# Performance work log

Hardware: AMD Instinct MI355X
Metric: run time of the kernel (lower is better)

Reference implementation:

```python
import jax, jax.numpy as jnp
import numpy as np

G = 8           # graphs
NBG = 1024      # blocks per graph
APB = 4         # atoms per block
NC = 1          # coord channels
HID = 512
ES = 64
K = 9
L = 3
NLVL = 50
NB = G * NBG
NU = NB * APB
NUM_BLOCK, NUM_ATOM, NUM_POS = 25, 16, 16
BIG = 1e9


def _cumsum_ids(seg_lengths, n):
    # faithful to torch: zeros, mark segment starts via cumsum(lengths)[:-1], cumsum
    ids = jnp.zeros((n,), jnp.int32).at[jnp.cumsum(seg_lengths)[:-1]].set(1)
    return jnp.cumsum(ids)


def setup_inputs() -> dict:
    key = jax.random.key(0)
    ks = jax.random.split(key, 18)
    s = 0.02
    return {
        'Z': 3.0 * jax.random.normal(ks[0], (NU, NC, 3), jnp.float32),
        'B': jax.random.randint(ks[1], (NB,), 0, NUM_BLOCK),
        'A': jax.random.randint(ks[2], (NU,), 0, NUM_ATOM),
        'atom_positions': jax.random.randint(ks[3], (NU,), 0, NUM_POS),
        'block_lengths': jnp.full((NB,), APB, jnp.int32),
        'lengths': jnp.full((G,), NBG, jnp.int32),
        'segment_ids': jax.random.randint(ks[4], (NB,), 0, 2),
        'noise': jax.random.normal(ks[5], (NU, NC, 3), jnp.float32),
        'noise_level': jax.random.randint(ks[6], (G,), 0, NLVL),
        'sigmas': jnp.asarray(np.exp(np.linspace(np.log(10.0), np.log(0.01), NLVL)), jnp.float32),
        'atom_emb': s * jax.random.normal(ks[7], (NUM_ATOM, HID), jnp.float32),
        'pos_emb': s * jax.random.normal(ks[8], (NUM_POS, HID), jnp.float32),
        'block_emb': s * jax.random.normal(ks[9], (NUM_BLOCK, HID), jnp.float32),
        'edge_emb': s * jax.random.normal(ks[10], (2, ES), jnp.float32),
        'Wm': s * jax.random.normal(ks[11], (L, HID, HID), jnp.float32),
        'We': s * jax.random.normal(ks[12], (L, ES, HID), jnp.float32),
        'Wu': s * jax.random.normal(ks[13], (L, HID, HID), jnp.float32),
        'wz': s * jax.random.normal(ks[14], (L, HID), jnp.float32),
        'W1': s * jax.random.normal(ks[15], (HID, HID), jnp.float32),
        'b1': jnp.zeros((HID,), jnp.float32),
        'W2': s * jax.random.normal(ks[16], (HID, 1), jnp.float32),
    }


def _forward(Z, B, A, atom_positions, block_lengths, lengths, segment_ids,
             noise, noise_level, sigmas, atom_emb, pos_emb, block_emb, edge_emb,
             Wm, We, Wu, wz, W1, b1, W2):
    nb, nu, g = B.shape[0], A.shape[0], lengths.shape[0]
    nbg, apb = nb // g, nu // nb
    batch_id = _cumsum_ids(lengths, nb)        # [Nb]
    block_id = _cumsum_ids(block_lengths, nu)  # [Nu]

    # perturb: Z + noise * sigma[noise_level[graph]]
    used = sigmas[noise_level][batch_id][block_id]          # [Nu]
    Zp = Z + noise * used[:, None, None]                    # [Nu, NC, 3]

    # block embedding: atom + position + block-type
    H0 = atom_emb[A] + pos_emb[atom_positions] + block_emb[B][block_id]  # [Nu, H]

    # edges: fully connect -> split intra/inter by segment -> knn by min atom-pair distance
    xa = Zp.reshape(g, nbg * apb * NC, 3)
    sq = jnp.sum(xa * xa, axis=-1)
    d2 = sq[:, :, None] + sq[:, None, :] - 2.0 * jnp.einsum('gnd,gmd->gnm', xa, xa)
    D = d2.reshape(g, nbg, apb * NC, nbg, apb * NC).min(axis=(2, 4))     # [g, nbg, nbg]
    seg = segment_ids.reshape(g, nbg)
    same = seg[:, :, None] == seg[:, None, :]
    eye = jnp.eye(nbg, dtype=bool)[None]
    _, idx_intra = jax.lax.top_k(-jnp.where(same & ~eye, D, BIG), K)     # [g, nbg, K]
    _, idx_inter = jax.lax.top_k(-jnp.where(~same, D, BIG), K)
    off = (jnp.arange(g, dtype=jnp.int32) * nbg)[:, None, None]
    dst_loc = jnp.broadcast_to(jnp.arange(nbg, dtype=jnp.int32)[None, :, None] + off, (g, nbg, K))
    src = jnp.concatenate([(idx_intra + off).reshape(-1), (idx_inter + off).reshape(-1)])
    dst = jnp.concatenate([dst_loc.reshape(-1), dst_loc.reshape(-1)])
    eattr = edge_emb[jnp.concatenate([jnp.zeros(g * nbg * K, jnp.int32), jnp.ones(g * nbg * K, jnp.int32)])]

    # encoder (GET surrogate): block-level equivariant message passing
    h = jax.ops.segment_sum(H0, block_id, num_segments=nb) / apb                    # [Nb, H]
    Zb0 = jax.ops.segment_sum(Zp.mean(axis=1), block_id, num_segments=nb) / apb    # [Nb, 3]
    Zb = Zb0
    for l in range(Wm.shape[0]):
        m = jax.nn.silu((h[src] + h[dst]) @ Wm[l] + eattr @ We[l])                  # [E, H]
        h = h + jax.nn.silu(jax.ops.segment_sum(m, dst, num_segments=nb) @ Wu[l])
        coef = jnp.tanh(m @ wz[l])                                                  # [E]
        Zb = Zb + jax.ops.segment_sum((Zb[src] - Zb[dst]) * coef[:, None], dst, num_segments=nb) / (2 * K)
    pred_Z = Zp + (Zb - Zb0)[block_id][:, None, :]
    unit_repr = H0 + h[block_id]
    block_repr = h
    graph_repr = jax.ops.segment_sum(h, batch_id, num_segments=g)

    # energy head: SiLU -> Linear -> SiLU -> Linear(no bias), summed per graph
    e = jax.nn.silu(jax.nn.silu(block_repr) @ W1 + b1) @ W2                         # [Nb, 1]
    pred_energy = jax.ops.segment_sum(e[:, 0], batch_id, num_segments=g)            # [g]

    pred_noise = pred_Z - Zp
    per_unit = jnp.sum((pred_noise - noise) ** 2, axis=(-1, -2))                    # [Nu]
    nl = jax.ops.segment_sum(per_unit, batch_id[block_id], num_segments=g)
    loss = 0.5 * nl.mean()
    return pred_energy, pred_noise, unit_repr, block_repr, graph_repr, loss


def reference(Z, B, A, atom_positions, block_lengths, lengths, segment_ids,
              noise, noise_level, sigmas, atom_emb, pos_emb, block_emb, edge_emb,
              Wm, We, Wu, wz, W1, b1, W2):
    return _forward(Z, B, A, atom_positions, block_lengths, lengths, segment_ids,
                    noise, noise_level, sigmas, atom_emb, pos_emb, block_emb, edge_emb,
                    Wm, We, Wu, wz, W1, b1, W2)
```

## Files before the change

kernel.cpp:

```cpp
#include <hip/hip_runtime.h>
#include <hip/hip_bf16.h>

typedef __bf16 bf16;
typedef __bf16 bf16x2 __attribute__((ext_vector_type(2)));
typedef __bf16 bf16x8 __attribute__((ext_vector_type(8)));
typedef float floatx4 __attribute__((ext_vector_type(4)));

#define NB_ 8192
#define NU_ 32768

__device__ __forceinline__ float silu_f(float x) {
    float e = __expf(-x);
    return x * __builtin_amdgcn_rcpf(1.0f + e);
}

__device__ __forceinline__ float2 unpack_bf2(unsigned v) {
    float2 r;
    r.x = __uint_as_float(v << 16);
    r.y = __uint_as_float(v & 0xFFFF0000u);
    return r;
}

__device__ __forceinline__ void gll16(const bf16* g, bf16* l) {
    __builtin_amdgcn_global_load_lds((const __attribute__((address_space(1))) void*)g,
                                     (__attribute__((address_space(3))) void*)l, 16, 0, 0);
}

__global__ __launch_bounds__(256) void init_kernel(
    const float* __restrict__ Z, const float* __restrict__ noise,
    const int* __restrict__ nl, const float* __restrict__ sig,
    const int* __restrict__ Aarr, const int* __restrict__ posa, const int* __restrict__ Barr,
    const float* __restrict__ atom_emb, const float* __restrict__ pos_emb,
    const float* __restrict__ block_emb,
    const float* __restrict__ edge_emb, const float* __restrict__ We,
    const float* __restrict__ Wm, const float* __restrict__ Wu, const float* __restrict__ W1,
    float* __restrict__ Zp, float* __restrict__ Zb0, float* __restrict__ Zb,
    float* __restrict__ hf, bf16* __restrict__ hb,
    bf16* __restrict__ WmT, bf16* __restrict__ WuT, bf16* __restrict__ W1T,
    float* __restrict__ ebias,
    float* __restrict__ out_gr, float* __restrict__ out_e, float* __restrict__ out_loss)
{
    __shared__ float zsh[12];
    __shared__ float tile[32][33];
    int bid = blockIdx.x, tid = threadIdx.x;
    if (bid < 8192) {
        int b = bid, g = b >> 10;
        if (tid < 12) {
            float sg = sig[nl[g]];
            int idx = b*12 + tid;
            float zp = Z[idx] + noise[idx]*sg;
            Zp[idx] = zp;
            zsh[tid] = zp;
        }
        __syncthreads();
        if (tid < 3) {
            float v = 0.25f*(zsh[tid] + zsh[3+tid] + zsh[6+tid] + zsh[9+tid]);
            Zb0[b*3+tid] = v; Zb[b*3+tid] = v;
        }
        int ai[4], pi[4];
        #pragma unroll
        for (int a = 0; a < 4; a++) { ai[a] = Aarr[b*4+a]*512; pi[a] = posa[b*4+a]*512; }
        int bb = Barr[b]*512;
        int c0 = tid*2;
        float sx = 0.0f, sy = 0.0f;
        #pragma unroll
        for (int a = 0; a < 4; a++) {
            float2 va = *(const float2*)(atom_emb + ai[a] + c0);
            float2 vp = *(const float2*)(pos_emb + pi[a] + c0);
            sx += va.x + vp.x; sy += va.y + vp.y;
        }
        float2 vb = *(const float2*)(block_emb + bb + c0);
        sx = 0.25f*sx + vb.x; sy = 0.25f*sy + vb.y;
        *(float2*)(hf + (size_t)b*512 + c0) = make_float2(sx, sy);
        bf16x2 hp = { (bf16)sx, (bf16)sy };
        *(bf16x2*)(hb + (size_t)b*512 + c0) = hp;
        return;
    }
    bid -= 8192;
    if (bid < 1792) {
        int z = bid >> 8, rem = bid & 255;
        int bx = rem & 15, by = rem >> 4;
        int tx = tid & 31, ty = tid >> 5;
        const float* src; bf16* dst;
        if (z < 3)      { src = Wm + (size_t)z*262144;     dst = WmT + (size_t)z*262144; }
        else if (z < 6) { src = Wu + (size_t)(z-3)*262144; dst = WuT + (size_t)(z-3)*262144; }
        else            { src = W1;                        dst = W1T; }
        #pragma unroll
        for (int i = 0; i < 32; i += 8)
            tile[ty+i][tx] = src[(size_t)(by*32+ty+i)*512 + bx*32+tx];
        __syncthreads();
        #pragma unroll
        for (int i = 0; i < 32; i += 8)
            dst[(size_t)(bx*32+ty+i)*512 + by*32+tx] = (bf16)tile[tx][ty+i];
        return;
    }
    bid -= 1792;
    if (bid < 12) {
        int gid = bid*256 + tid;
        int l = gid >> 10, t = (gid >> 9) & 1, c = gid & 511;
        float s = 0.0f;
        #pragma unroll 8
        for (int e = 0; e < 64; e++)
            s += edge_emb[t*64 + e] * We[(size_t)(l*64 + e)*512 + c];
        ebias[gid] = s;
        return;
    }
    bid -= 12;
    int k = bid*256 + tid;
    if (k < 4096) out_gr[k] = 0.0f;
    else if (k < 4104) out_e[k-4096] = 0.0f;
    else if (k == 4104) out_loss[0] = 0.0f;
}

__device__ void knn_body(int kb, const float* __restrict__ Zp, const int* __restrict__ seg,
                         int* __restrict__ nbr, unsigned* __restrict__ l1) {
    int tid = threadIdx.x, w = tid >> 6, lane = tid & 63;
    int g = kb & 7, rl = kb >> 3;
    int r = (g << 10) + rl;
    int base = g << 10;
    int segr = seg[r];
    const float4* zp4 = (const float4*)(Zp + (size_t)r*12);
    float4 a0 = zp4[0], a1 = zp4[1], a2 = zp4[2];
    float ax[4] = {a0.x, a0.w, a1.z, a2.y};
    float ay[4] = {a0.y, a1.x, a1.w, a2.z};
    float az[4] = {a0.z, a1.y, a2.x, a2.w};
    unsigned kin[4], kout[4];
    #pragma unroll
    for (int t = 0; t < 4; t++) {
        int j = w*256 + t*64 + lane;
        int jb = base + j;
        const float4* p = (const float4*)(Zp + (size_t)jb*12);
        float4 v0 = p[0], v1 = p[1], v2 = p[2];
        float bx[4] = {v0.x, v0.w, v1.z, v2.y};
        float by[4] = {v0.y, v1.x, v1.w, v2.z};
        float bz[4] = {v0.z, v1.y, v2.x, v2.w};
        float dm = 3.0e38f;
        #pragma unroll
        for (int a = 0; a < 4; a++) {
            #pragma unroll
            for (int bq = 0; bq < 4; bq++) {
                float dx = ax[a]-bx[bq], dy = ay[a]-by[bq], dz = az[a]-bz[bq];
                dm = fminf(dm, dx*dx + dy*dy + dz*dz);
            }
        }
        unsigned kd = (__float_as_uint(dm) & 0xFFFFFC00u) | (unsigned)j;
        bool same = (seg[jb] == segr);
        kin[t]  = (same && j != rl) ? kd : 0xFFFFFFFFu;
        kout[t] = (!same)           ? kd : 0xFFFFFFFFu;
    }
    if (tid < 128) l1[tid] = 0xFFFFFFFFu;
    __syncthreads();
    #pragma unroll
    for (int ph = 0; ph < 2; ph++) {
        unsigned wd[4];
        #pragma unroll
        for (int t = 0; t < 4; t++) wd[t] = ph ? kout[t] : kin[t];
        for (int it = 0; it < 9; it++) {
            unsigned bk = min(min(wd[0], wd[1]), min(wd[2], wd[3]));
            unsigned mv = bk;
            #pragma unroll
            for (int off = 32; off >= 1; off >>= 1)
                mv = min(mv, (unsigned)__shfl_xor((int)mv, off, 64));
            if (lane == 0) l1[ph*64 + w*16 + it] = mv;
            if (bk == mv) {
                #pragma unroll
                for (int t = 0; t < 4; t++) if (wd[t] == mv) wd[t] = 0xFFFFFFFFu;
            }
        }
    }
    __syncthreads();
    if (w < 2) {
        int ph = w;
        int w2 = lane >> 4, it2 = lane & 15;
        unsigned key = (it2 < 9) ? l1[ph*64 + w2*16 + it2] : 0xFFFFFFFFu;
        for (int it = 0; it < 9; it++) {
            unsigned mv = key;
            #pragma unroll
            for (int off = 32; off >= 1; off >>= 1)
                mv = min(mv, (unsigned)__shfl_xor((int)mv, off, 64));
            if (key == mv) key = 0xFFFFFFFFu;
            if (lane == 0) nbr[r*18 + ph*9 + it] = base + (int)(mv & 1023u);
        }
    }
}

__device__ void gemm_body(const bf16* __restrict__ A, const bf16* __restrict__ BT,
                          bf16* __restrict__ Pb, float* __restrict__ hf,
                          bf16* __restrict__ hb, bf16* __restrict__ shp,
                          const float* __restrict__ b1, const float* __restrict__ W2,
                          float* __restrict__ out_e,
                          float* __restrict__ Zb, const float* __restrict__ zacc,
                          int mode, int bid, bf16* __restrict__ sA, bf16* __restrict__ sB)
{
    int mt = bid & 127, nt = bid >> 7;
    int m0 = mt*64, n0 = nt*64;
    int tid = threadIdx.x, lane = tid & 63, w = tid >> 6;
    int wm = w & 1, wn = w >> 1;
    int lm = lane & 15, q = lane >> 4;

    int row = tid >> 2;
    int qt = (tid & 3) ^ ((row >> 1) & 3);
    const bf16* gA = A  + (size_t)(m0 + row)*512 + qt*8;
    const bf16* gB = BT + (size_t)(n0 + row)*512 + qt*8;
    bf16* lA = sA + tid*8 - lane*8;
    bf16* lB = sB + tid*8 - lane*8;
    int swq = (q ^ ((lm >> 1) & 3)) * 8;

    floatx4 zv = {0.0f, 0.0f, 0.0f, 0.0f};
    floatx4 acc[2][2];
    #pragma unroll
    for (int i = 0; i < 2; i++)
        #pragma unroll
        for (int j = 0; j < 2; j++) acc[i][j] = zv;

    gll16(gA, lA);
    gll16(gB, lB);
    for (int k = 0; k < 16; k++) {
        int cur = (k & 1)*2048;
        __syncthreads();
        if (k < 15) {
            int nxt = ((k+1) & 1)*2048;
            gll16(gA + (k+1)*32, lA + nxt);
            gll16(gB + (k+1)*32, lB + nxt);
        }
        const bf16* bA = sA + cur;
        const bf16* bB = sB + cur;
        bf16x8 af[2], bfr[2];
        af[0]  = *(const bf16x8*)(bA + (wm*32      + lm)*32 + swq);
        af[1]  = *(const bf16x8*)(bA + (wm*32 + 16 + lm)*32 + swq);
        bfr[0] = *(const bf16x8*)(bB + (wn*32      + lm)*32 + swq);
        bfr[1] = *(const bf16x8*)(bB + (wn*32 + 16 + lm)*32 + swq);
        #pragma unroll
        for (int tm = 0; tm < 2; tm++)
            #pragma unroll
            for (int tn = 0; tn < 2; tn++)
                acc[tm][tn] = __builtin_amdgcn_mfma_f32_16x16x32_bf16(af[tm], bfr[tn], acc[tm][tn], 0, 0, 0);
    }

    if (mode == 2) {
        float s = 0.0f;
        #pragma unroll
        for (int tn = 0; tn < 2; tn++) {
            int col = n0 + wn*32 + tn*16 + lm;
            float bb = b1[col], ww = W2[col];
            #pragma unroll
            for (int tm = 0; tm < 2; tm++)
                #pragma unroll
                for (int rr = 0; rr < 4; rr++)
                    s += silu_f(acc[tm][tn][rr] + bb) * ww;
        }
        #pragma unroll
        for (int off = 32; off >= 1; off >>= 1) s += __shfl_xor(s, off, 64);
        if (lane == 0) atomicAdd(&out_e[m0 >> 10], s);
        return;
    }
    if (mode == 1 && nt == 0 && tid < 192) {
        int o = m0*3 + tid;
        Zb[o] += zacc[o] * (1.0f/18.0f);
    }
    #pragma unroll
    for (int tm = 0; tm < 2; tm++) {
        #pragma unroll
        for (int tn = 0; tn < 2; tn++) {
            #pragma unroll
            for (int rr = 0; rr < 4; rr++) {
                int r2 = m0 + wm*32 + tm*16 + q*4 + rr;
                int c2 = n0 + wn*32 + tn*16 + lm;
                size_t o = (size_t)r2*512 + c2;
                float v = acc[tm][tn][rr];
                if (mode == 0) {
                    Pb[o] = (bf16)v;
                } else {
                    float nh = hf[o] + silu_f(v);
                    hf[o] = nh;
                    hb[o] = (bf16)nh;
                    if (shp) shp[o] = (bf16)silu_f(nh);
                }
            }
        }
    }
}

__global__ __launch_bounds__(256) void gemm_kernel(const bf16* __restrict__ A, const bf16* __restrict__ BT,
                                                   bf16* __restrict__ Pb, float* __restrict__ hf,
                                                   bf16* __restrict__ hb, bf16* __restrict__ shp,
                                                   float* __restrict__ Zb, const float* __restrict__ zacc,
                                                   int mode) {
    __shared__ __align__(16) char smem[16384];
    gemm_body(A, BT, Pb, hf, hb, shp, nullptr, nullptr, nullptr, Zb, zacc, mode, blockIdx.x,
              (bf16*)smem, (bf16*)(smem + 8192));
}

__global__ __launch_bounds__(256) void knn_pgemm0_kernel(const bf16* __restrict__ hb,
                                                         const bf16* __restrict__ WmT0,
                                                         bf16* __restrict__ Pb,
                                                         const float* __restrict__ Zp,
                                                         const int* __restrict__ seg,
                                                         int* __restrict__ nbr) {
    __shared__ __align__(16) char smem[16384];
    if (blockIdx.x < 8192)
        knn_body(blockIdx.x, Zp, seg, nbr, (unsigned*)smem);
    else
        gemm_body(hb, WmT0, Pb, nullptr, nullptr, nullptr, nullptr, nullptr, nullptr,
                  nullptr, nullptr, 0, blockIdx.x - 8192, (bf16*)smem, (bf16*)(smem + 8192));
}

__global__ __launch_bounds__(256) void edge_kernel(const bf16* __restrict__ Pb, const float* __restrict__ ebias,
                                                   const float* __restrict__ wz, const float* __restrict__ Zb,
                                                   const int* __restrict__ nbr, bf16* __restrict__ msum,
                                                   float* __restrict__ zacc) {
    int bid = blockIdx.x, tid = threadIdx.x;
    int b = ((bid & 7) << 10) | (bid >> 3);
    int c0 = 2*tid;
    int lane = tid & 63, wid = tid >> 6;
    __shared__ int srcs[18];
    __shared__ float red[18][4];
    __shared__ float term[18][3];
    if (tid < 18) srcs[tid] = nbr[b*18 + tid];
    __syncthreads();
    float2 pd  = unpack_bf2(*(const unsigned*)(Pb + (size_t)b*512 + c0));
    float2 eb0 = *(const float2*)(ebias + c0);
    float2 eb1 = *(const float2*)(ebias + 512 + c0);
    float2 w   = *(const float2*)(wz + c0);
    float ms0 = 0.0f, ms1 = 0.0f;
    float pdot[18];
    #pragma unroll
    for (int e = 0; e < 18; e++) {
        int s = srcs[e];
        float2 pv = unpack_bf2(*(const unsigned*)(Pb + (size_t)s*512 + c0));
        float ba = (e < 9) ? eb0.x : eb1.x;
        float bb = (e < 9) ? eb0.y : eb1.y;
        float m0 = silu_f(pv.x + pd.x + ba);
        float m1 = silu_f(pv.y + pd.y + bb);
        ms0 += m0; ms1 += m1;
        pdot[e] = m0*w.x + m1*w.y;
    }
    bf16x2 mp = { (bf16)ms0, (bf16)ms1 };
    *(bf16x2*)(msum + (size_t)b*512 + c0) = mp;
    #pragma unroll
    for (int e = 0; e < 18; e++) {
        float v = pdot[e];
        #pragma unroll
        for (int off = 32; off >= 1; off >>= 1) v += __shfl_xor(v, off, 64);
        if (lane == 0) red[e][wid] = v;
    }
    __syncthreads();
    if (tid < 18) {
        float dot = red[tid][0] + red[tid][1] + red[tid][2] + red[tid][3];
        float coef = tanhf(dot);
        int s = srcs[tid];
        #pragma unroll
        for (int d = 0; d < 3; d++)
            term[tid][d] = (Zb[s*3 + d] - Zb[b*3 + d]) * coef;
    }
    __syncthreads();
    if (tid < 3) {
        float s = 0.0f;
        #pragma unroll
        for (int e = 0; e < 18; e++) s += term[e][tid];
        zacc[b*3 + tid] = s;
    }
}

__global__ __launch_bounds__(256) void egemm_fin_kernel(const bf16* __restrict__ sh, const bf16* __restrict__ W1T,
                                                        const float* __restrict__ b1, const float* __restrict__ W2,
                                                        float* __restrict__ out_e,
                                                        const float* __restrict__ hf, float* __restrict__ out_gr,
                                                        const float* __restrict__ Zb, const float* __restrict__ Zb0,
                                                        const float* __restrict__ noise,
                                                        float* __restrict__ out_pn, float* __restrict__ out_loss) {
    __shared__ __align__(16) char smem[16384];
    int bid = blockIdx.x, tid = threadIdx.x;
    if (bid < 1024) {
        gemm_body(sh, W1T, nullptr, nullptr, nullptr, nullptr, b1, W2, out_e,
                  nullptr, nullptr, 2, bid, (bf16*)smem, (bf16*)(smem + 8192));
        return;
    }
    float* red = (float*)smem;
    if (bid < 1152) {
        int u = (bid-1024)*256 + tid;
        int b = u >> 2;
        float per = 0.0f;
        #pragma unroll
        for (int d = 0; d < 3; d++) {
            float dv = Zb[b*3+d] - Zb0[b*3+d];
            out_pn[u*3+d] = dv;
            float e = dv - noise[u*3+d];
            per += e*e;
        }
        red[tid] = per; __syncthreads();
        for (int st = 128; st > 0; st >>= 1) {
            if (tid < st) red[tid] += red[tid+st];
            __syncthreads();
        }
        if (tid == 0) atomicAdd(out_loss, red[0] * (1.0f/16.0f));
        return;
    }
    int pid = bid - 1152;
    int g = pid >> 5;
    int rc = (pid >> 1) & 15;
    int ch = pid & 1;
    int c = ch*256 + tid;
    int b0 = (g << 10) + rc*64;
    float s = 0.0f;
    for (int i = 0; i < 64; i++) s += hf[(size_t)(b0+i)*512 + c];
    atomicAdd(&out_gr[g*512 + c], s);
}

__global__ __launch_bounds__(256) void unitrepr_kernel(const int* __restrict__ Aarr, const int* __restrict__ posa,
                                                       const int* __restrict__ Barr,
                                                       const float* __restrict__ atom_emb, const float* __restrict__ pos_emb,
                                                       const float* __restrict__ block_emb,
                                                       const float* __restrict__ hf, float* __restrict__ out_ur) {
    int gid = blockIdx.x*256 + threadIdx.x;
    int u = gid >> 7, c = (gid & 127) << 2, b = u >> 2;
    float4 va = *(const float4*)(atom_emb + (size_t)Aarr[u]*512 + c);
    float4 vp = *(const float4*)(pos_emb + (size_t)posa[u]*512 + c);
    float4 vb = *(const float4*)(block_emb + (size_t)Barr[b]*512 + c);
    float4 vh = *(const float4*)(hf + (size_t)b*512 + c);
    float4 o;
    o.x = va.x + vp.x + vb.x + vh.x;
    o.y = va.y + vp.y + vb.y + vh.y;
    o.z = va.z + vp.z + vb.z + vh.z;
    o.w = va.w + vp.w + vb.w + vh.w;
    *(float4*)(out_ur + (size_t)u*512 + c) = o;
}

extern "C" void kernel_launch(void* const* d_in, const int* in_sizes, int n_in,
                              void* d_out, int out_size, void* d_ws, size_t ws_size,
                              hipStream_t stream) {
    const float* Z         = (const float*)d_in[0];
    const int*   B         = (const int*)d_in[1];
    const int*   A         = (const int*)d_in[2];
    const int*   ap        = (const int*)d_in[3];
    const int*   seg       = (const int*)d_in[6];
    const float* noise     = (const float*)d_in[7];
    const int*   nl        = (const int*)d_in[8];
    const float* sig       = (const float*)d_in[9];
    const float* atom_emb  = (const float*)d_in[10];
    const float* pos_emb   = (const float*)d_in[11];
    const float* block_emb = (const float*)d_in[12];
    const float* edge_emb  = (const float*)d_in[13];
    const float* Wm        = (const float*)d_in[14];
    const float* We        = (const float*)d_in[15];
    const float* Wu        = (const float*)d_in[16];
    const float* wz        = (const float*)d_in[17];
    const float* W1        = (const float*)d_in[18];
    const float* b1        = (const float*)d_in[19];
    const float* W2        = (const float*)d_in[20];
    (void)in_sizes; (void)n_in; (void)d_ws; (void)ws_size; (void)out_size;

    float* out = (float*)d_out;
    const size_t o1 = 8, o2 = 98312, o3 = 16875528, o4 = 21069832, o5 = 21073928;
    float* out_e    = out;
    float* out_pn   = out + o1;
    float* out_ur   = out + o2;
    float* hf       = out + o3;
    float* out_gr   = out + o4;
    float* out_loss = out + o5;

    char* arena = (char*)(out + o2);
    bf16*  Pb   = (bf16*)(arena);
    bf16*  msum = (bf16*)(arena + 16777216);
    bf16*  sh   = (bf16*)(arena + 25165824);
    bf16*  hb   = (bf16*)(arena + 33554432);
    float* Zp   = (float*)(arena + 41943040);
    float* Zb0  = (float*)(arena + 42336256);
    float* Zb   = (float*)(arena + 42434560);
    float* zacc = (float*)(arena + 42532864);
    int*   nbr  = (int*)  (arena + 42631168);
    bf16*  WmT  = (bf16*) (arena + 43220992);
    bf16*  WuT  = (bf16*) (arena + 44793856);
    bf16*  W1T  = (bf16*) (arena + 46366720);
    float* ebias= (float*)(arena + 46891008);

    init_kernel<<<8192 + 1792 + 12 + 17, 256, 0, stream>>>(
        Z, noise, nl, sig, A, ap, B, atom_emb, pos_emb, block_emb,
        edge_emb, We, Wm, Wu, W1,
        Zp, Zb0, Zb, hf, hb, WmT, WuT, W1T, ebias, out_gr, out_e, out_loss);

    knn_pgemm0_kernel<<<8192 + 1024, 256, 0, stream>>>(hb, WmT, Pb, Zp, seg, nbr);

    for (int l = 0; l < 3; l++) {
        if (l > 0)
            gemm_kernel<<<1024, 256, 0, stream>>>(hb, WmT + (size_t)l*262144, Pb,
                                                  nullptr, nullptr, nullptr, nullptr, nullptr, 0);
        edge_kernel<<<8192, 256, 0, stream>>>(Pb, ebias + l*1024, wz + l*512, Zb, nbr, msum, zacc);
        gemm_kernel<<<1024, 256, 0, stream>>>(msum, WuT + (size_t)l*262144, nullptr,
                                              hf, hb, (l == 2) ? sh : nullptr, Zb, zacc, 1);
    }
    egemm_fin_kernel<<<1024 + 128 + 256, 256, 0, stream>>>(sh, W1T, b1, W2, out_e,
                                                           hf, out_gr, Zb, Zb0, noise, out_pn, out_loss);
    unitrepr_kernel<<<16384, 256, 0, stream>>>(A, ap, B, atom_emb, pos_emb, block_emb, hf, out_ur);
}
```

Measured before the change: 530.2 us.

## Batch eight KNN queries per block and enlarge GEMM tile to 128x64

The KNN kernel now handles eight destination blocks per workgroup. Each candidate's coordinates and segment id are loaded once and reused across all eight queries, with distance keys and same-segment ballots staged in shared memory before each wave runs a top-9 selection for two queries. The GEMM body moves from a 64x64 to a 128x64 output tile, which halves the block count and improves operand reuse. In exchange it drops the double-buffered global-to-LDS prefetch for a single buffer with two barriers per k step, and it needs more registers and a larger shared allocation in the KNN kernel.

```diff
diff --git a/kernel.cpp b/kernel.cpp
--- a/kernel.cpp
+++ b/kernel.cpp
@@ -112,74 +112,94 @@
     else if (k == 4104) out_loss[0] = 0.0f;
 }
 
-__device__ void knn_body(int kb, const float* __restrict__ Zp, const int* __restrict__ seg,
-                         int* __restrict__ nbr, unsigned* __restrict__ l1) {
+__device__ void knn_body8(int kb, const float* __restrict__ Zp, const int* __restrict__ seg,
+                          int* __restrict__ nbr, char* __restrict__ smem) {
+    unsigned* keys = (unsigned*)smem;
+    unsigned* smk  = (unsigned*)(smem + 32768);
+    float*    dza  = (float*)(smem + 33792);
+    int*      sseg = (int*)(smem + 34176);
     int tid = threadIdx.x, w = tid >> 6, lane = tid & 63;
-    int g = kb & 7, rl = kb >> 3;
-    int r = (g << 10) + rl;
+    int g = kb & 7, grp = kb >> 3;
     int base = g << 10;
-    int segr = seg[r];
-    const float4* zp4 = (const float4*)(Zp + (size_t)r*12);
-    float4 a0 = zp4[0], a1 = zp4[1], a2 = zp4[2];
-    float ax[4] = {a0.x, a0.w, a1.z, a2.y};
-    float ay[4] = {a0.y, a1.x, a1.w, a2.z};
-    float az[4] = {a0.z, a1.y, a2.x, a2.w};
-    unsigned kin[4], kout[4];
+    int dst0 = grp << 3;
+    if (tid < 96) dza[tid] = Zp[(size_t)(base + dst0)*12 + tid];
+    if (tid < 8)  sseg[tid] = seg[base + dst0 + tid];
+    __syncthreads();
+    float sx[4][4], sy[4][4], sz[4][4]; int sj[4];
     #pragma unroll
     for (int t = 0; t < 4; t++) {
         int j = w*256 + t*64 + lane;
-        int jb = base + j;
-        const float4* p = (const float4*)(Zp + (size_t)jb*12);
+        const float4* p = (const float4*)(Zp + (size_t)(base + j)*12);
         float4 v0 = p[0], v1 = p[1], v2 = p[2];
-        float bx[4] = {v0.x, v0.w, v1.z, v2.y};
-        float by[4] = {v0.y, v1.x, v1.w, v2.z};
-        float bz[4] = {v0.z, v1.y, v2.x, v2.w};
-        float dm = 3.0e38f;
-        #pragma unroll
-        for (int a = 0; a < 4; a++) {
+        sx[t][0]=v0.x; sx[t][1]=v0.w; sx[t][2]=v1.z; sx[t][3]=v2.y;
+        sy[t][0]=v0.y; sy[t][1]=v1.x; sy[t][2]=v1.w; sy[t][3]=v2.z;
+        sz[t][0]=v0.z; sz[t][1]=v1.y; sz[t][2]=v2.x; sz[t][3]=v2.w;
+        sj[t] = seg[base + j];
+    }
+    #pragma unroll
+    for (int d = 0; d < 8; d++) {
+        const float4* ap4 = (const float4*)(dza + d*12);
+        float4 a0 = ap4[0], a1 = ap4[1], a2 = ap4[2];
+        float ax[4] = {a0.x, a0.w, a1.z, a2.y};
+        float ay[4] = {a0.y, a1.x, a1.w, a2.z};
+        float az[4] = {a0.z, a1.y, a2.x, a2.w};
+        int segd = sseg[d];
+        int dl = dst0 + d;
+        #pragma unroll
+        for (int t = 0; t < 4; t++) {
+            int j = w*256 + t*64 + lane;
+            float dm = 3.0e38f;
             #pragma unroll
-            for (int bq = 0; bq < 4; bq++) {
-                float dx = ax[a]-bx[bq], dy = ay[a]-by[bq], dz = az[a]-bz[bq];
-                dm = fminf(dm, dx*dx + dy*dy + dz*dz);
+            for (int a = 0; a < 4; a++) {
+                #pragma unroll
+                for (int bq = 0; bq < 4; bq++) {
+                    float dx = ax[a]-sx[t][bq], dy = ay[a]-sy[t][bq], dz = az[a]-sz[t][bq];
+                    dm = fminf(dm, dx*dx + dy*dy + dz*dz);
+                }
             }
-        }
-        unsigned kd = (__float_as_uint(dm) & 0xFFFFFC00u) | (unsigned)j;
-        bool same = (seg[jb] == segr);
-        kin[t]  = (same && j != rl) ? kd : 0xFFFFFFFFu;
-        kout[t] = (!same)           ? kd : 0xFFFFFFFFu;
-    }
-    if (tid < 128) l1[tid] = 0xFFFFFFFFu;
+            unsigned key = (__float_as_uint(dm) & 0xFFFFFC00u) | (unsigned)j;
+            if (j == dl) key = 0xFFFFFFFFu;
+            bool same = (sj[t] == segd);
+            unsigned long long bal = __ballot(same);
+            if (lane == 0) {
+                smk[d*32 + (w*4+t)*2]     = (unsigned)bal;
+                smk[d*32 + (w*4+t)*2 + 1] = (unsigned)(bal >> 32);
+            }
+            keys[d*1024 + j] = key;
+        }
+    }
     __syncthreads();
     #pragma unroll
-    for (int ph = 0; ph < 2; ph++) {
-        unsigned wd[4];
-        #pragma unroll
-        for (int t = 0; t < 4; t++) wd[t] = ph ? kout[t] : kin[t];
-        for (int it = 0; it < 9; it++) {
-            unsigned bk = min(min(wd[0], wd[1]), min(wd[2], wd[3]));
-            unsigned mv = bk;
+    for (int half = 0; half < 2; half++) {
+        int d = w + half*4;
+        int r = base + dst0 + d;
+        unsigned kk[16], sm[16];
+        #pragma unroll
+        for (int t2 = 0; t2 < 16; t2++) {
+            kk[t2] = keys[d*1024 + t2*64 + lane];
+            unsigned wrd = smk[d*32 + t2*2 + (lane >> 5)];
+            sm[t2] = (wrd >> (lane & 31)) & 1u;
+        }
+        #pragma unroll
+        for (int ph = 0; ph < 2; ph++) {
+            unsigned wd[16];
             #pragma unroll
-            for (int off = 32; off >= 1; off >>= 1)
-                mv = min(mv, (unsigned)__shfl_xor((int)mv, off, 64));
-            if (lane == 0) l1[ph*64 + w*16 + it] = mv;
-            if (bk == mv) {
+            for (int t2 = 0; t2 < 16; t2++)
+                wd[t2] = (ph == 0) ? (sm[t2] ? kk[t2] : 0xFFFFFFFFu)
+                                   : (sm[t2] ? 0xFFFFFFFFu : kk[t2]);
+            for (int it = 0; it < 9; it++) {
+                unsigned bk = wd[0];
                 #pragma unroll
-                for (int t = 0; t < 4; t++) if (wd[t] == mv) wd[t] = 0xFFFFFFFFu;
+                for (int t2 = 1; t2 < 16; t2++) bk = min(bk, wd[t2]);
+                unsigned mv = bk;
+                #pragma unroll
+                for (int off = 32; off >= 1; off >>= 1)
+                    mv = min(mv, (unsigned)__shfl_xor((int)mv, off, 64));
+                if (lane == 0) nbr[r*18 + ph*9 + it] = base + (int)(mv & 1023u);
+                #pragma unroll
+                for (int t2 = 0; t2 < 16; t2++)
+                    wd[t2] = (wd[t2] == mv) ? 0xFFFFFFFFu : wd[t2];
             }
-        }
-    }
-    __syncthreads();
-    if (w < 2) {
-        int ph = w;
-        int w2 = lane >> 4, it2 = lane & 15;
-        unsigned key = (it2 < 9) ? l1[ph*64 + w2*16 + it2] : 0xFFFFFFFFu;
-        for (int it = 0; it < 9; it++) {
-            unsigned mv = key;
-            #pragma unroll
-            for (int off = 32; off >= 1; off >>= 1)
-                mv = min(mv, (unsigned)__shfl_xor((int)mv, off, 64));
-            if (key == mv) key = 0xFFFFFFFFu;
-            if (lane == 0) nbr[r*18 + ph*9 + it] = base + (int)(mv & 1023u);
         }
     }
 }
@@ -192,49 +212,53 @@
                           float* __restrict__ Zb, const float* __restrict__ zacc,
                           int mode, int bid, bf16* __restrict__ sA, bf16* __restrict__ sB)
 {
-    int mt = bid & 127, nt = bid >> 7;
-    int m0 = mt*64, n0 = nt*64;
+    int mt = bid & 63, nt = bid >> 6;
+    int m0 = mt*128, n0 = nt*64;
     int tid = threadIdx.x, lane = tid & 63, w = tid >> 6;
     int wm = w & 1, wn = w >> 1;
     int lm = lane & 15, q = lane >> 4;
 
-    int row = tid >> 2;
-    int qt = (tid & 3) ^ ((row >> 1) & 3);
-    const bf16* gA = A  + (size_t)(m0 + row)*512 + qt*8;
-    const bf16* gB = BT + (size_t)(n0 + row)*512 + qt*8;
-    bf16* lA = sA + tid*8 - lane*8;
-    bf16* lB = sB + tid*8 - lane*8;
+    int pA0 = w*128 + lane, pA1 = pA0 + 64, pB = w*64 + lane;
+    int rA0 = pA0 >> 2, qA0 = (pA0 & 3) ^ ((rA0 >> 1) & 3);
+    int rA1 = pA1 >> 2, qA1 = (pA1 & 3) ^ ((rA1 >> 1) & 3);
+    int rB  = pB  >> 2, qB  = (pB  & 3) ^ ((rB  >> 1) & 3);
+    const bf16* gA0 = A  + (size_t)(m0 + rA0)*512 + qA0*8;
+    const bf16* gA1 = A  + (size_t)(m0 + rA1)*512 + qA1*8;
+    const bf16* gB  = BT + (size_t)(n0 + rB )*512 + qB*8;
+    bf16* lA0 = sA + (w*128)*8;
+    bf16* lA1 = sA + (w*128 + 64)*8;
+    bf16* lB  = sB + (w*64)*8;
+
     int swq = (q ^ ((lm >> 1) & 3)) * 8;
+    const bf16* pa[4]; const bf16* pb2[2];
+    #pragma unroll
+    for (int tm = 0; tm < 4; tm++) pa[tm] = sA + (wm*64 + tm*16 + lm)*32 + swq;
+    #pragma unroll
+    for (int tn = 0; tn < 2; tn++) pb2[tn] = sB + (wn*32 + tn*16 + lm)*32 + swq;
 
     floatx4 zv = {0.0f, 0.0f, 0.0f, 0.0f};
-    floatx4 acc[2][2];
-    #pragma unroll
-    for (int i = 0; i < 2; i++)
+    floatx4 acc[4][2];
+    #pragma unroll
+    for (int i = 0; i < 4; i++)
         #pragma unroll
         for (int j = 0; j < 2; j++) acc[i][j] = zv;
 
-    gll16(gA, lA);
-    gll16(gB, lB);
-    for (int k = 0; k < 16; k++) {
-        int cur = (k & 1)*2048;
+    for (int k0 = 0; k0 < 512; k0 += 32) {
+        gll16(gA0 + k0, lA0);
+        gll16(gA1 + k0, lA1);
+        gll16(gB  + k0, lB);
         __syncthreads();
-        if (k < 15) {
-            int nxt = ((k+1) & 1)*2048;
-            gll16(gA + (k+1)*32, lA + nxt);
-            gll16(gB + (k+1)*32, lB + nxt);
-        }
-        const bf16* bA = sA + cur;
-        const bf16* bB = sB + cur;
-        bf16x8 af[2], bfr[2];
-        af[0]  = *(const bf16x8*)(bA + (wm*32      + lm)*32 + swq);
-        af[1]  = *(const bf16x8*)(bA + (wm*32 + 16 + lm)*32 + swq);
-        bfr[0] = *(const bf16x8*)(bB + (wn*32      + lm)*32 + swq);
-        bfr[1] = *(const bf16x8*)(bB + (wn*32 + 16 + lm)*32 + swq);
-        #pragma unroll
-        for (int tm = 0; tm < 2; tm++)
+        bf16x8 af[4], bfr[2];
+        #pragma unroll
+        for (int tm = 0; tm < 4; tm++) af[tm] = *(const bf16x8*)pa[tm];
+        #pragma unroll
+        for (int tn = 0; tn < 2; tn++) bfr[tn] = *(const bf16x8*)pb2[tn];
+        #pragma unroll
+        for (int tm = 0; tm < 4; tm++)
             #pragma unroll
             for (int tn = 0; tn < 2; tn++)
                 acc[tm][tn] = __builtin_amdgcn_mfma_f32_16x16x32_bf16(af[tm], bfr[tn], acc[tm][tn], 0, 0, 0);
+        __syncthreads();
     }
 
     if (mode == 2) {
@@ -244,7 +268,7 @@
             int col = n0 + wn*32 + tn*16 + lm;
             float bb = b1[col], ww = W2[col];
             #pragma unroll
-            for (int tm = 0; tm < 2; tm++)
+            for (int tm = 0; tm < 4; tm++)
                 #pragma unroll
                 for (int rr = 0; rr < 4; rr++)
                     s += silu_f(acc[tm][tn][rr] + bb) * ww;
@@ -254,17 +278,21 @@
         if (lane == 0) atomicAdd(&out_e[m0 >> 10], s);
         return;
     }
-    if (mode == 1 && nt == 0 && tid < 192) {
+    if (mode == 1 && nt == 0) {
         int o = m0*3 + tid;
         Zb[o] += zacc[o] * (1.0f/18.0f);
-    }
-    #pragma unroll
-    for (int tm = 0; tm < 2; tm++) {
+        if (tid < 128) {
+            int o2 = m0*3 + 256 + tid;
+            Zb[o2] += zacc[o2] * (1.0f/18.0f);
+        }
+    }
+    #pragma unroll
+    for (int tm = 0; tm < 4; tm++) {
         #pragma unroll
         for (int tn = 0; tn < 2; tn++) {
             #pragma unroll
             for (int rr = 0; rr < 4; rr++) {
-                int r2 = m0 + wm*32 + tm*16 + q*4 + rr;
+                int r2 = m0 + wm*64 + tm*16 + q*4 + rr;
                 int c2 = n0 + wn*32 + tn*16 + lm;
                 size_t o = (size_t)r2*512 + c2;
                 float v = acc[tm][tn][rr];
@@ -286,7 +314,7 @@
                                                    bf16* __restrict__ hb, bf16* __restrict__ shp,
                                                    float* __restrict__ Zb, const float* __restrict__ zacc,
                                                    int mode) {
-    __shared__ __align__(16) char smem[16384];
+    __shared__ __align__(16) char smem[12288];
     gemm_body(A, BT, Pb, hf, hb, shp, nullptr, nullptr, nullptr, Zb, zacc, mode, blockIdx.x,
               (bf16*)smem, (bf16*)(smem + 8192));
 }
@@ -297,12 +325,12 @@
                                                          const float* __restrict__ Zp,
                                                          const int* __restrict__ seg,
                                                          int* __restrict__ nbr) {
-    __shared__ __align__(16) char smem[16384];
-    if (blockIdx.x < 8192)
-        knn_body(blockIdx.x, Zp, seg, nbr, (unsigned*)smem);
+    __shared__ __align__(16) char smem[34240];
+    if (blockIdx.x < 1024)
+        knn_body8(blockIdx.x, Zp, seg, nbr, smem);
     else
         gemm_body(hb, WmT0, Pb, nullptr, nullptr, nullptr, nullptr, nullptr, nullptr,
-                  nullptr, nullptr, 0, blockIdx.x - 8192, (bf16*)smem, (bf16*)(smem + 8192));
+                  nullptr, nullptr, 0, blockIdx.x - 1024, (bf16*)smem, (bf16*)(smem + 8192));
 }
 
 __global__ __launch_bounds__(256) void edge_kernel(const bf16* __restrict__ Pb, const float* __restrict__ ebias,
@@ -369,16 +397,16 @@
                                                         const float* __restrict__ Zb, const float* __restrict__ Zb0,
                                                         const float* __restrict__ noise,
                                                         float* __restrict__ out_pn, float* __restrict__ out_loss) {
-    __shared__ __align__(16) char smem[16384];
+    __shared__ __align__(16) char smem[12288];
     int bid = blockIdx.x, tid = threadIdx.x;
-    if (bid < 1024) {
+    if (bid < 512) {
         gemm_body(sh, W1T, nullptr, nullptr, nullptr, nullptr, b1, W2, out_e,
                   nullptr, nullptr, 2, bid, (bf16*)smem, (bf16*)(smem + 8192));
         return;
     }
     float* red = (float*)smem;
-    if (bid < 1152) {
-        int u = (bid-1024)*256 + tid;
+    if (bid < 640) {
+        int u = (bid-512)*256 + tid;
         int b = u >> 2;
         float per = 0.0f;
         #pragma unroll
@@ -396,7 +424,7 @@
         if (tid == 0) atomicAdd(out_loss, red[0] * (1.0f/16.0f));
         return;
     }
-    int pid = bid - 1152;
+    int pid = bid - 640;
     int g = pid >> 5;
     int rc = (pid >> 1) & 15;
     int ch = pid & 1;
@@ -479,17 +507,17 @@
         edge_emb, We, Wm, Wu, W1,
         Zp, Zb0, Zb, hf, hb, WmT, WuT, W1T, ebias, out_gr, out_e, out_loss);
 
-    knn_pgemm0_kernel<<<8192 + 1024, 256, 0, stream>>>(hb, WmT, Pb, Zp, seg, nbr);
+    knn_pgemm0_kernel<<<1024 + 512, 256, 0, stream>>>(hb, WmT, Pb, Zp, seg, nbr);
 
     for (int l = 0; l < 3; l++) {
         if (l > 0)
-            gemm_kernel<<<1024, 256, 0, stream>>>(hb, WmT + (size_t)l*262144, Pb,
-                                                  nullptr, nullptr, nullptr, nullptr, nullptr, 0);
+            gemm_kernel<<<512, 256, 0, stream>>>(hb, WmT + (size_t)l*262144, Pb,
+                                                 nullptr, nullptr, nullptr, nullptr, nullptr, 0);
         edge_kernel<<<8192, 256, 0, stream>>>(Pb, ebias + l*1024, wz + l*512, Zb, nbr, msum, zacc);
-        gemm_kernel<<<1024, 256, 0, stream>>>(msum, WuT + (size_t)l*262144, nullptr,
-                                              hf, hb, (l == 2) ? sh : nullptr, Zb, zacc, 1);
-    }
-    egemm_fin_kernel<<<1024 + 128 + 256, 256, 0, stream>>>(sh, W1T, b1, W2, out_e,
-                                                           hf, out_gr, Zb, Zb0, noise, out_pn, out_loss);
+        gemm_kernel<<<512, 256, 0, stream>>>(msum, WuT + (size_t)l*262144, nullptr,
+                                             hf, hb, (l == 2) ? sh : nullptr, Zb, zacc, 1);
+    }
+    egemm_fin_kernel<<<512 + 128 + 256, 256, 0, stream>>>(sh, W1T, b1, W2, out_e,
+                                                          hf, out_gr, Zb, Zb0, noise, out_pn, out_loss);
     unitrepr_kernel<<<16384, 256, 0, stream>>>(A, ap, B, atom_emb, pos_emb, block_emb, hf, out_ur);
 }
```

Result: faster. 487.2 us (-8.1%).
